# Optimization experiments

Measured on AMD Instinct MI355X. Metric: run time of the kernel, lower is better.

The kernel has to match this reference:

```python
import jax, jax.numpy as jnp
import numpy as np

S = 9                      # spiral length
V = [8192, 4096, 2048, 1024, 512]  # verts per level, finest -> latent


def grid_sample_bilinear(feat, grid):
    # feat [B,C,H,W], grid [B,P,2] in [-1,1]; bilinear, align_corners=True
    B, C, H, W = feat.shape
    x = (grid[..., 0] + 1.0) * 0.5 * (W - 1)
    y = (grid[..., 1] + 1.0) * 0.5 * (H - 1)
    x0 = jnp.floor(x); y0 = jnp.floor(y)
    wx = x - x0; wy = y - y0
    x0i = jnp.clip(x0.astype(jnp.int32), 0, W - 1)
    x1i = jnp.clip(x0.astype(jnp.int32) + 1, 0, W - 1)
    y0i = jnp.clip(y0.astype(jnp.int32), 0, H - 1)
    y1i = jnp.clip(y0.astype(jnp.int32) + 1, 0, H - 1)
    featf = feat.reshape(B, C, H * W).transpose(0, 2, 1)  # [B,HW,C]
    def gat(yi, xi):
        return jnp.take_along_axis(featf, (yi * W + xi)[..., None], axis=1)  # [B,P,C]
    w00 = ((1 - wy) * (1 - wx))[..., None]
    w01 = ((1 - wy) * wx)[..., None]
    w10 = (wy * (1 - wx))[..., None]
    w11 = (wy * wx)[..., None]
    return gat(y0i, x0i) * w00 + gat(y0i, x1i) * w01 + gat(y1i, x0i) * w10 + gat(y1i, x1i) * w11


def pool(x, row, col, val):
    # sparse mesh upsample: gather cols, scale, scatter-add into rows
    n_out = row.shape[0] // 3
    g = x[:, col, :] * val[None, :, None]                       # [B,nnz,C]
    return jnp.zeros((x.shape[0], n_out, x.shape[-1]), x.dtype).at[:, row, :].add(g)


def dsconv(x, idx, wd, wp, b):
    # depthwise-separable spiral conv: gather spiral ring, depthwise over S, pointwise mix
    g = x[:, idx]                                # [B,N,S,C]
    dw = jnp.einsum('bnsc,sc->bnc', g, wd)       # depthwise over spiral dim
    return jnp.einsum('bnc,co->bno', dw, wp) + b # pointwise


def _forward(uv, feat, upsample, s0, s1, s2, s3,
             row0, col0, val0, row1, col1, val1, row2, col2, val2, row3, col3, val3,
             wd0, wp0, b0, wd1, wp1, b1, wd2, wp2, b2, wd3, wp3, b3, wdh, wph, bh):
    uvc = jnp.clip((uv - 0.5) * 2.0, -1.0, 1.0)
    x = grid_sample_bilinear(feat, uvc)           # [B,P,C]  (torch: [B,C,P] then permute)
    x = jnp.einsum('vp,bpc->bvc', upsample, x)    # [B,V4,C] latent mesh features
    x = jax.nn.relu(dsconv(pool(x, row3, col3, val3), s3, wd0, wp0, b0))  # [B,1024,512]
    x = jax.nn.relu(dsconv(pool(x, row2, col2, val2), s2, wd1, wp1, b1))  # [B,2048,256]
    x = jax.nn.relu(dsconv(pool(x, row1, col1, val1), s1, wd2, wp2, b2))  # [B,4096,128]
    x = jax.nn.relu(dsconv(pool(x, row0, col0, val0), s0, wd3, wp3, b3))  # [B,8192,64]
    return dsconv(x, s0, wdh, wph, bh)            # [B,8192,3]


def setup_inputs():
    ks = jax.random.split(jax.random.key(0), 64)
    B, P, C, H, W = 8, 21, 512, 32, 32
    inp = {}
    inp['uv'] = jax.random.uniform(ks[0], (B, P, 2), jnp.float32)
    inp['feat'] = jax.random.normal(ks[1], (B, C, H, W), jnp.float32)
    inp['upsample'] = 0.01 * jnp.ones((V[4], P), jnp.float32)
    for i in range(4):
        inp[f's{i}'] = jax.random.randint(ks[2 + i], (V[i], S), 0, V[i])
    for i in range(4):
        nnz = 3 * V[i]
        inp[f'row{i}'] = jax.random.randint(ks[6 + 3 * i], (nnz,), 0, V[i])
        inp[f'col{i}'] = jax.random.randint(ks[7 + 3 * i], (nnz,), 0, V[i + 1])
        inp[f'val{i}'] = jax.random.uniform(ks[8 + 3 * i], (nnz,), jnp.float32)
    chans = [(512, 512), (512, 256), (256, 128), (128, 64), (64, 3)]
    names = ['0', '1', '2', '3', 'h']
    k = 20
    for (ci, co), nm in zip(chans, names):
        inp[f'wd{nm}'] = 0.1 * jax.random.normal(ks[k], (S, ci), jnp.float32); k += 1
        inp[f'wp{nm}'] = jax.random.normal(ks[k], (ci, co), jnp.float32) * (1.0 / float(np.sqrt(ci))); k += 1
        inp[f'b{nm}'] = jnp.zeros((co,), jnp.float32); k += 1
    return inp


def reference(uv, feat, upsample, s0, s1, s2, s3,
              row0, col0, val0, row1, col1, val1, row2, col2, val2, row3, col3, val3,
              wd0, wp0, b0, wd1, wp1, b1, wd2, wp2, b2, wd3, wp3, b3, wdh, wph, bh):
    return _forward(uv, feat, upsample, s0, s1, s2, s3,
                    row0, col0, val0, row1, col1, val1, row2, col2, val2, row3, col3, val3,
                    wd0, wp0, b0, wd1, wp1, b1, wd2, wp2, b2, wd3, wp3, b3, wdh, wph, bh)
```

## Files before the change

### kernel.cpp

```cpp
#include <hip/hip_runtime.h>

#define B_  8
#define P_  21
#define H_  32
#define W_  32

typedef float f32x4 __attribute__((ext_vector_type(4)));
typedef _Float16 f16x8 __attribute__((ext_vector_type(8)));

struct CsrParams {
  const int*   row[4];
  const int*   col[4];
  const float* val[4];
  int*   cnt[4];
  int*   rowptr[4];
  int*   colsout[4];
  float* valsout[4];
  int    nnz[4];
  int    V[4];
};

__global__ void count_kernel(CsrParams p) {
  int l = blockIdx.y;
  int k = blockIdx.x * 256 + threadIdx.x;
  if (k < p.nnz[l]) atomicAdd(&p.cnt[l][p.row[l][k]], 1);
}

__global__ void scan_kernel(CsrParams p) {
  int l = blockIdx.x;
  int V = p.V[l];
  int* cnt = p.cnt[l];
  int* rp  = p.rowptr[l];
  int t = threadIdx.x;
  int chunk = V / 256;
  int base = t * chunk;
  int s = 0;
  for (int i = 0; i < chunk; ++i) s += cnt[base + i];
  __shared__ int sm[256];
  sm[t] = s;
  __syncthreads();
  for (int off = 1; off < 256; off <<= 1) {
    int v = (t >= off) ? sm[t - off] : 0;
    __syncthreads();
    sm[t] += v;
    __syncthreads();
  }
  int run = sm[t] - s;
  for (int i = 0; i < chunk; ++i) {
    int c = cnt[base + i];
    rp[base + i]  = run;
    cnt[base + i] = run;
    run += c;
  }
  if (t == 255) rp[V] = run;
}

__global__ void fill_kernel(CsrParams p) {
  int l = blockIdx.y;
  int k = blockIdx.x * 256 + threadIdx.x;
  if (k < p.nnz[l]) {
    int r = p.row[l][k];
    int pos = atomicAdd(&p.cnt[l][r], 1);
    p.colsout[l][pos] = p.col[l][k];
    p.valsout[l][pos] = p.val[l][k];
  }
}

__global__ void sample_kernel(const float* __restrict__ uv,
                              const float* __restrict__ feat,
                              float* __restrict__ xs) {
  int bp = blockIdx.x;
  int b  = bp / P_;
  float u0 = uv[bp * 2 + 0], u1 = uv[bp * 2 + 1];
  float gx = fminf(fmaxf((u0 - 0.5f) * 2.0f, -1.0f), 1.0f);
  float gy = fminf(fmaxf((u1 - 0.5f) * 2.0f, -1.0f), 1.0f);
  float fx = (gx + 1.0f) * 0.5f * (W_ - 1);
  float fy = (gy + 1.0f) * 0.5f * (H_ - 1);
  float x0f = floorf(fx), y0f = floorf(fy);
  float wx = fx - x0f, wy = fy - y0f;
  int x0 = (int)x0f, y0 = (int)y0f;
  int x0i = min(max(x0, 0), W_ - 1), x1i = min(max(x0 + 1, 0), W_ - 1);
  int y0i = min(max(y0, 0), H_ - 1), y1i = min(max(y0 + 1, 0), H_ - 1);
  float w00 = (1.f - wy) * (1.f - wx), w01 = (1.f - wy) * wx;
  float w10 = wy * (1.f - wx),        w11 = wy * wx;
  for (int c = threadIdx.x; c < 512; c += blockDim.x) {
    const float* fb = feat + ((size_t)(b * 512 + c)) * (H_ * W_);
    float v = fb[y0i * W_ + x0i] * w00 + fb[y0i * W_ + x1i] * w01 +
              fb[y1i * W_ + x0i] * w10 + fb[y1i * W_ + x1i] * w11;
    xs[(size_t)bp * 512 + c] = v;
  }
}

__global__ void upsample_kernel(const float* __restrict__ up,
                                const float* __restrict__ xs,
                                float* __restrict__ xu) {
  int v = blockIdx.x, b = blockIdx.y;
  int c4 = threadIdx.x << 2;
  float4 acc = make_float4(0.f, 0.f, 0.f, 0.f);
  for (int p = 0; p < P_; ++p) {
    float u = up[v * P_ + p];
    const float4 xv = *(const float4*)&xs[((size_t)(b * P_ + p)) * 512 + c4];
    acc.x = fmaf(u, xv.x, acc.x);
    acc.y = fmaf(u, xv.y, acc.y);
    acc.z = fmaf(u, xv.z, acc.z);
    acc.w = fmaf(u, xv.w, acc.w);
  }
  *(float4*)&xu[((size_t)(b * 512 + v)) * 512 + c4] = acc;
}

__global__ __launch_bounds__(256) void pool_kernel(
    const float* __restrict__ x,
    const int* __restrict__ rowptr,
    const int* __restrict__ cols,
    const float* __restrict__ vals,
    float* __restrict__ out,
    int Vout, int Vin, int Cin) {
  const int lpr    = Cin >> 3;
  const int lshift = 31 - __clz(lpr);
  const int rpb    = 256 >> lshift;
  const int lr = threadIdx.x >> lshift;
  const int lc = threadIdx.x & (lpr - 1);
  const int b  = blockIdx.x & 7;
  const int n  = (blockIdx.x >> 3) * rpb + lr;
  const int c8 = lc << 3;
  const float* xb = x + (size_t)b * Vin * Cin + c8;
  int j0 = rowptr[n], j1 = rowptr[n + 1];
  float4 a0 = make_float4(0.f, 0.f, 0.f, 0.f);
  float4 a1 = make_float4(0.f, 0.f, 0.f, 0.f);
  for (int j = j0; j < j1; ++j) {
    float v = vals[j];
    const float* xr = xb + (size_t)cols[j] * Cin;
    float4 x0 = *(const float4*)xr;
    float4 x1 = *(const float4*)(xr + 4);
    a0.x = fmaf(v, x0.x, a0.x); a0.y = fmaf(v, x0.y, a0.y);
    a0.z = fmaf(v, x0.z, a0.z); a0.w = fmaf(v, x0.w, a0.w);
    a1.x = fmaf(v, x1.x, a1.x); a1.y = fmaf(v, x1.y, a1.y);
    a1.z = fmaf(v, x1.z, a1.z); a1.w = fmaf(v, x1.w, a1.w);
  }
  float* op = &out[((size_t)b * Vout + n) * Cin + c8];
  *(float4*)op = a0;
  *(float4*)(op + 4) = a1;
}

__global__ __launch_bounds__(256) void dw_split_kernel(
    const float* __restrict__ xin,
    const int* __restrict__ sidx,
    const float* __restrict__ wd,
    _Float16* __restrict__ a0o,
    _Float16* __restrict__ a1o,
    int Vout, int Cin) {
  const int lpr    = Cin >> 3;
  const int lshift = 31 - __clz(lpr);
  const int rpb    = 256 >> lshift;
  const int lr = threadIdx.x >> lshift;
  const int lc = threadIdx.x & (lpr - 1);
  const int b  = blockIdx.x & 7;
  const int n  = (blockIdx.x >> 3) * rpb + lr;
  const int c8 = lc << 3;
  const float* xb = xin + (size_t)b * Vout * Cin + c8;

  int idx[9];
  #pragma unroll
  for (int s = 0; s < 9; ++s) idx[s] = sidx[n * 9 + s];

  float4 a0 = make_float4(0.f, 0.f, 0.f, 0.f);
  float4 a1 = make_float4(0.f, 0.f, 0.f, 0.f);
  #pragma unroll
  for (int s = 0; s < 9; ++s) {
    const float* xr = xb + (size_t)idx[s] * Cin;
    float4 x0 = *(const float4*)xr;
    float4 x1 = *(const float4*)(xr + 4);
    const float* wr = wd + s * Cin + c8;
    float4 w0 = *(const float4*)wr;
    float4 w1 = *(const float4*)(wr + 4);
    a0.x = fmaf(w0.x, x0.x, a0.x); a0.y = fmaf(w0.y, x0.y, a0.y);
    a0.z = fmaf(w0.z, x0.z, a0.z); a0.w = fmaf(w0.w, x0.w, a0.w);
    a1.x = fmaf(w1.x, x1.x, a1.x); a1.y = fmaf(w1.y, x1.y, a1.y);
    a1.z = fmaf(w1.z, x1.z, a1.z); a1.w = fmaf(w1.w, x1.w, a1.w);
  }

  size_t m = (size_t)b * Vout + n;
  float v[8] = {a0.x, a0.y, a0.z, a0.w, a1.x, a1.y, a1.z, a1.w};
  f16x8 hi, lo;
  #pragma unroll
  for (int i = 0; i < 8; ++i) {
    _Float16 h0 = (_Float16)v[i];
    float r = (v[i] - (float)h0) * 2048.0f;
    hi[i] = h0;
    lo[i] = (_Float16)r;
  }
  *(f16x8*)&a0o[m * Cin + c8] = hi;
  *(f16x8*)&a1o[m * Cin + c8] = lo;
}

struct BsplitParams {
  const float* wp[4];
  int K[4], N[4], off[4];
  _Float16* b0;
  _Float16* b1;
};

__global__ void bsplit_all_kernel(BsplitParams p) {
  int idx = blockIdx.x * 256 + threadIdx.x;
  #pragma unroll
  for (int t = 0; t < 4; ++t) {
    int sz = p.N[t] * p.K[t];
    if (idx < sz) {
      int n = idx / p.K[t], k = idx - n * p.K[t];
      float v = p.wp[t][(size_t)k * p.N[t] + n];
      _Float16 h0 = (_Float16)v;
      float r = (v - (float)h0) * 2048.0f;
      p.b0[p.off[t] + idx] = h0;
      p.b1[p.off[t] + idx] = (_Float16)r;
      return;
    }
    idx -= sz;
  }
}

__global__ __launch_bounds__(256) void gemm_f16x2(
    const _Float16* __restrict__ A0, const _Float16* __restrict__ A1,
    const _Float16* __restrict__ Bt0, const _Float16* __restrict__ Bt1,
    const float* __restrict__ bias, float* __restrict__ C,
    int M, int N, int K) {
  constexpr int RP = 72;
  __shared__ _Float16 As[2][128][RP];
  __shared__ _Float16 Bs[2][64][RP];
  const int tid = threadIdx.x;
  const int bx = blockIdx.x;
  const int xr_ = (bx & 7) * (gridDim.x >> 3) + (bx >> 3);
  const int m0 = xr_ * 128, n0 = blockIdx.y * 64;
  const int wid = tid >> 6, lane = tid & 63;
  const int wr = wid >> 1, wc = wid & 1;
  const int lo = lane & 15, hi = lane >> 4;

  f32x4 accM[4][2], accC[4][2];
  #pragma unroll
  for (int mi = 0; mi < 4; ++mi)
    #pragma unroll
    for (int nj = 0; nj < 2; ++nj) {
      accM[mi][nj] = (f32x4){0.f, 0.f, 0.f, 0.f};
      accC[mi][nj] = (f32x4){0.f, 0.f, 0.f, 0.f};
    }

  const _Float16* gA[2] = {A0, A1};
  const _Float16* gB[2] = {Bt0, Bt1};

  for (int k0 = 0; k0 < K; k0 += 64) {
    #pragma unroll
    for (int p = 0; p < 2; ++p) {
      #pragma unroll
      for (int i = 0; i < 4; ++i) {
        int c = tid + 256 * i;
        int r = c >> 3, k8 = (c & 7) << 3;
        uint4 v = *(const uint4*)(gA[p] + (size_t)(m0 + r) * K + k0 + k8);
        *(uint4*)&As[p][r][k8] = v;
      }
      #pragma unroll
      for (int i = 0; i < 2; ++i) {
        int c = tid + 256 * i;
        int r = c >> 3, k8 = (c & 7) << 3;
        uint4 v = *(const uint4*)(gB[p] + (size_t)(n0 + r) * K + k0 + k8);
        *(uint4*)&Bs[p][r][k8] = v;
      }
    }
    __syncthreads();
    #pragma unroll
    for (int s = 0; s < 2; ++s) {
      const int kk = s * 32 + hi * 8;
      f16x8 af[4][2], bf[2][2];
      #pragma unroll
      for (int mi = 0; mi < 4; ++mi) {
        af[mi][0] = *(const f16x8*)&As[0][wr * 64 + mi * 16 + lo][kk];
        af[mi][1] = *(const f16x8*)&As[1][wr * 64 + mi * 16 + lo][kk];
      }
      #pragma unroll
      for (int nj = 0; nj < 2; ++nj) {
        bf[nj][0] = *(const f16x8*)&Bs[0][wc * 32 + nj * 16 + lo][kk];
        bf[nj][1] = *(const f16x8*)&Bs[1][wc * 32 + nj * 16 + lo][kk];
      }
      #pragma unroll
      for (int mi = 0; mi < 4; ++mi)
        #pragma unroll
        for (int nj = 0; nj < 2; ++nj) {
          accM[mi][nj] = __builtin_amdgcn_mfma_f32_16x16x32_f16(
              af[mi][0], bf[nj][0], accM[mi][nj], 0, 0, 0);
          accC[mi][nj] = __builtin_amdgcn_mfma_f32_16x16x32_f16(
              af[mi][0], bf[nj][1], accC[mi][nj], 0, 0, 0);
          accC[mi][nj] = __builtin_amdgcn_mfma_f32_16x16x32_f16(
              af[mi][1], bf[nj][0], accC[mi][nj], 0, 0, 0);
        }
    }
    __syncthreads();
  }

  const float INV = 1.0f / 2048.0f;
  #pragma unroll
  for (int mi = 0; mi < 4; ++mi)
    #pragma unroll
    for (int nj = 0; nj < 2; ++nj) {
      int col = n0 + wc * 32 + nj * 16 + lo;
      float bv = bias[col];
      #pragma unroll
      for (int r = 0; r < 4; ++r) {
        int row = m0 + wr * 64 + mi * 16 + hi * 4 + r;
        float v = accM[mi][nj][r] + accC[mi][nj][r] * INV + bv;
        v = fmaxf(v, 0.f);
        C[(size_t)row * N + col] = v;
      }
    }
}

__global__ __launch_bounds__(256) void head_fused_kernel(
    const float* __restrict__ x,
    const int* __restrict__ sidx,
    const float* __restrict__ wdh,
    const float* __restrict__ wph,
    const float* __restrict__ bh,
    float* __restrict__ out) {
  const int bid  = blockIdx.x;
  const int b    = bid & 7;
  const int wid  = threadIdx.x >> 6;
  const int lane = threadIdx.x & 63;
  const int n    = (bid >> 3) * 4 + wid;
  const float* xb = x + (size_t)b * 8192 * 64 + lane;

  int idx[9];
  #pragma unroll
  for (int s = 0; s < 9; ++s) idx[s] = sidx[n * 9 + s];

  float acc = 0.f;
  #pragma unroll
  for (int s = 0; s < 9; ++s)
    acc = fmaf(wdh[s * 64 + lane], xb[(size_t)idx[s] * 64], acc);

  float a0 = acc * wph[lane * 3 + 0];
  float a1 = acc * wph[lane * 3 + 1];
  float a2 = acc * wph[lane * 3 + 2];
  for (int off = 32; off > 0; off >>= 1) {
    a0 += __shfl_down(a0, off);
    a1 += __shfl_down(a1, off);
    a2 += __shfl_down(a2, off);
  }
  if (lane == 0) {
    size_t row = (size_t)b * 8192 + n;
    out[row * 3 + 0] = a0 + bh[0];
    out[row * 3 + 1] = a1 + bh[1];
    out[row * 3 + 2] = a2 + bh[2];
  }
}

extern "C" void kernel_launch(void* const* d_in, const int* in_sizes, int n_in,
                              void* d_out, int out_size, void* d_ws, size_t ws_size,
                              hipStream_t stream) {
  const float* uv   = (const float*)d_in[0];
  const float* feat = (const float*)d_in[1];
  const float* up   = (const float*)d_in[2];
  const int* sArr[4] = {(const int*)d_in[3], (const int*)d_in[4],
                        (const int*)d_in[5], (const int*)d_in[6]};

  const size_t SLAB = 8ull * 2048 * 512;
  float* Wf = (float*)d_ws;
  float* S0 = Wf;
  float* S1 = Wf + SLAB;
  _Float16* A0 = (_Float16*)(S1 + SLAB);
  _Float16* A1 = A0 + SLAB;
  _Float16* Bt0all = (_Float16*)(S0 + 4500000);
  _Float16* Bt1all = Bt0all + 434176;
  float* xs = (float*)(A1 + SLAB);
  int* ib = (int*)(xs + (size_t)B_ * P_ * 512);

  int Vt[4] = {1024, 2048, 4096, 8192};
  int NZ[4] = {3072, 6144, 12288, 24576};
  int* cnt[4]; int* rp[4]; int* co[4]; float* va[4];
  {
    int* pc = ib;
    for (int t = 0; t < 4; ++t) { cnt[t] = pc; pc += Vt[t]; }
    for (int t = 0; t < 4; ++t) { rp[t] = pc; pc += Vt[t] + 1; }
    for (int t = 0; t < 4; ++t) { co[t] = pc; pc += NZ[t]; }
    float* pv = (float*)pc;
    for (int t = 0; t < 4; ++t) { va[t] = pv; pv += NZ[t]; }
  }

  CsrParams cp;
  for (int t = 0; t < 4; ++t) {
    int i = 3 - t;
    cp.row[t] = (const int*)d_in[7 + 3 * i];
    cp.col[t] = (const int*)d_in[8 + 3 * i];
    cp.val[t] = (const float*)d_in[9 + 3 * i];
    cp.cnt[t] = cnt[t]; cp.rowptr[t] = rp[t];
    cp.colsout[t] = co[t]; cp.valsout[t] = va[t];
    cp.nnz[t] = NZ[t]; cp.V[t] = Vt[t];
  }

  hipMemsetAsync(ib, 0, 15360 * sizeof(int), stream);
  count_kernel<<<dim3(96, 4), 256, 0, stream>>>(cp);
  scan_kernel<<<4, 256, 0, stream>>>(cp);
  fill_kernel<<<dim3(96, 4), 256, 0, stream>>>(cp);

  sample_kernel<<<B_ * P_, 256, 0, stream>>>(uv, feat, xs);
  upsample_kernel<<<dim3(512, B_), 128, 0, stream>>>(up, xs, S0);

  struct Stg { int Vin, Vout, Cin, Cout; const int* s; const float *wd, *wp, *bias; };
  Stg st[4] = {
    {512, 1024, 512, 512, sArr[3], (const float*)d_in[19], (const float*)d_in[20], (const float*)d_in[21]},
    {1024, 2048, 512, 256, sArr[2], (const float*)d_in[22], (const float*)d_in[23], (const float*)d_in[24]},
    {2048, 4096, 256, 128, sArr[1], (const float*)d_in[25], (const float*)d_in[26], (const float*)d_in[27]},
    {4096, 8192, 128, 64, sArr[0], (const float*)d_in[28], (const float*)d_in[29], (const float*)d_in[30]},
  };

  BsplitParams bp;
  int boff = 0;
  for (int t = 0; t < 4; ++t) {
    bp.wp[t] = st[t].wp;
    bp.K[t] = st[t].Cin; bp.N[t] = st[t].Cout;
    bp.off[t] = boff;
    boff += st[t].Cin * st[t].Cout;
  }
  bp.b0 = Bt0all; bp.b1 = Bt1all;
  bsplit_all_kernel<<<(boff + 255) / 256, 256, 0, stream>>>(bp);

  for (int t = 0; t < 4; ++t) {
    int rpb = 2048 / st[t].Cin;
    pool_kernel<<<8 * (st[t].Vout / rpb), 256, 0, stream>>>(
        S0, rp[t], co[t], va[t], S1, st[t].Vout, st[t].Vin, st[t].Cin);
    dw_split_kernel<<<8 * (st[t].Vout / rpb), 256, 0, stream>>>(
        S1, st[t].s, st[t].wd, A0, A1, st[t].Vout, st[t].Cin);
    int M = B_ * st[t].Vout;
    gemm_f16x2<<<dim3(M / 128, st[t].Cout / 64), 256, 0, stream>>>(
        A0, A1, Bt0all + bp.off[t], Bt1all + bp.off[t],
        st[t].bias, S0, M, st[t].Cout, st[t].Cin);
  }

  head_fused_kernel<<<8 * (8192 / 4), 256, 0, stream>>>(
      S0, sArr[0], (const float*)d_in[31], (const float*)d_in[32],
      (const float*)d_in[33], (float*)d_out);
}
```

Before: 280.1 us.

## Widen GEMM N-tile to 128 and process two vertices per thread in depthwise kernel

The GEMM is templated on its N-tile width. Layers with at least 128 output channels now use 128-wide tiles, so each loaded A tile is reused across more MFMAs, at the cost of more accumulator registers; launch bounds now request two blocks per CU. The depthwise split kernel handles two vertices per thread (n and n + Vout/2) with half the grid. This adds memory-level parallelism for the gathers but doubles register use per thread.

```diff
diff --git a/kernel.cpp b/kernel.cpp
--- a/kernel.cpp
+++ b/kernel.cpp
@@ -156,20 +156,28 @@
   const int lc = threadIdx.x & (lpr - 1);
   const int b  = blockIdx.x & 7;
   const int n  = (blockIdx.x >> 3) * rpb + lr;
+  const int n2 = n + (Vout >> 1);
   const int c8 = lc << 3;
   const float* xb = xin + (size_t)b * Vout * Cin + c8;
 
-  int idx[9];
-  #pragma unroll
-  for (int s = 0; s < 9; ++s) idx[s] = sidx[n * 9 + s];
+  int idx[9], idx2[9];
+  #pragma unroll
+  for (int s = 0; s < 9; ++s) idx[s]  = sidx[n * 9 + s];
+  #pragma unroll
+  for (int s = 0; s < 9; ++s) idx2[s] = sidx[n2 * 9 + s];
 
   float4 a0 = make_float4(0.f, 0.f, 0.f, 0.f);
   float4 a1 = make_float4(0.f, 0.f, 0.f, 0.f);
+  float4 c0 = make_float4(0.f, 0.f, 0.f, 0.f);
+  float4 c1 = make_float4(0.f, 0.f, 0.f, 0.f);
   #pragma unroll
   for (int s = 0; s < 9; ++s) {
-    const float* xr = xb + (size_t)idx[s] * Cin;
+    const float* xr  = xb + (size_t)idx[s]  * Cin;
+    const float* xr2 = xb + (size_t)idx2[s] * Cin;
     float4 x0 = *(const float4*)xr;
     float4 x1 = *(const float4*)(xr + 4);
+    float4 y0 = *(const float4*)xr2;
+    float4 y1 = *(const float4*)(xr2 + 4);
     const float* wr = wd + s * Cin + c8;
     float4 w0 = *(const float4*)wr;
     float4 w1 = *(const float4*)(wr + 4);
@@ -177,20 +185,30 @@
     a0.z = fmaf(w0.z, x0.z, a0.z); a0.w = fmaf(w0.w, x0.w, a0.w);
     a1.x = fmaf(w1.x, x1.x, a1.x); a1.y = fmaf(w1.y, x1.y, a1.y);
     a1.z = fmaf(w1.z, x1.z, a1.z); a1.w = fmaf(w1.w, x1.w, a1.w);
-  }
-
-  size_t m = (size_t)b * Vout + n;
-  float v[8] = {a0.x, a0.y, a0.z, a0.w, a1.x, a1.y, a1.z, a1.w};
-  f16x8 hi, lo;
+    c0.x = fmaf(w0.x, y0.x, c0.x); c0.y = fmaf(w0.y, y0.y, c0.y);
+    c0.z = fmaf(w0.z, y0.z, c0.z); c0.w = fmaf(w0.w, y0.w, c0.w);
+    c1.x = fmaf(w1.x, y1.x, c1.x); c1.y = fmaf(w1.y, y1.y, c1.y);
+    c1.z = fmaf(w1.z, y1.z, c1.z); c1.w = fmaf(w1.w, y1.w, c1.w);
+  }
+
+  size_t m  = (size_t)b * Vout + n;
+  size_t m2 = (size_t)b * Vout + n2;
+  float va[8] = {a0.x, a0.y, a0.z, a0.w, a1.x, a1.y, a1.z, a1.w};
+  float vc[8] = {c0.x, c0.y, c0.z, c0.w, c1.x, c1.y, c1.z, c1.w};
+  f16x8 hiA, loA, hiC, loC;
   #pragma unroll
   for (int i = 0; i < 8; ++i) {
-    _Float16 h0 = (_Float16)v[i];
-    float r = (v[i] - (float)h0) * 2048.0f;
-    hi[i] = h0;
-    lo[i] = (_Float16)r;
-  }
-  *(f16x8*)&a0o[m * Cin + c8] = hi;
-  *(f16x8*)&a1o[m * Cin + c8] = lo;
+    _Float16 h0 = (_Float16)va[i];
+    float r = (va[i] - (float)h0) * 2048.0f;
+    hiA[i] = h0; loA[i] = (_Float16)r;
+    _Float16 h1 = (_Float16)vc[i];
+    float r2 = (vc[i] - (float)h1) * 2048.0f;
+    hiC[i] = h1; loC[i] = (_Float16)r2;
+  }
+  *(f16x8*)&a0o[m  * Cin + c8] = hiA;
+  *(f16x8*)&a1o[m  * Cin + c8] = loA;
+  *(f16x8*)&a0o[m2 * Cin + c8] = hiC;
+  *(f16x8*)&a1o[m2 * Cin + c8] = loC;
 }
 
 struct BsplitParams {
@@ -218,27 +236,29 @@
   }
 }
 
-__global__ __launch_bounds__(256) void gemm_f16x2(
+template <int BN>
+__global__ __launch_bounds__(256, 2) void gemm_f16x2(
     const _Float16* __restrict__ A0, const _Float16* __restrict__ A1,
     const _Float16* __restrict__ Bt0, const _Float16* __restrict__ Bt1,
     const float* __restrict__ bias, float* __restrict__ C,
     int M, int N, int K) {
   constexpr int RP = 72;
+  constexpr int NR = BN / 32;
   __shared__ _Float16 As[2][128][RP];
-  __shared__ _Float16 Bs[2][64][RP];
+  __shared__ _Float16 Bs[2][BN][RP];
   const int tid = threadIdx.x;
   const int bx = blockIdx.x;
   const int xr_ = (bx & 7) * (gridDim.x >> 3) + (bx >> 3);
-  const int m0 = xr_ * 128, n0 = blockIdx.y * 64;
+  const int m0 = xr_ * 128, n0 = blockIdx.y * BN;
   const int wid = tid >> 6, lane = tid & 63;
   const int wr = wid >> 1, wc = wid & 1;
   const int lo = lane & 15, hi = lane >> 4;
 
-  f32x4 accM[4][2], accC[4][2];
+  f32x4 accM[4][NR], accC[4][NR];
   #pragma unroll
   for (int mi = 0; mi < 4; ++mi)
     #pragma unroll
-    for (int nj = 0; nj < 2; ++nj) {
+    for (int nj = 0; nj < NR; ++nj) {
       accM[mi][nj] = (f32x4){0.f, 0.f, 0.f, 0.f};
       accC[mi][nj] = (f32x4){0.f, 0.f, 0.f, 0.f};
     }
@@ -257,7 +277,7 @@
         *(uint4*)&As[p][r][k8] = v;
       }
       #pragma unroll
-      for (int i = 0; i < 2; ++i) {
+      for (int i = 0; i < BN / 32; ++i) {
         int c = tid + 256 * i;
         int r = c >> 3, k8 = (c & 7) << 3;
         uint4 v = *(const uint4*)(gB[p] + (size_t)(n0 + r) * K + k0 + k8);
@@ -268,21 +288,21 @@
     #pragma unroll
     for (int s = 0; s < 2; ++s) {
       const int kk = s * 32 + hi * 8;
-      f16x8 af[4][2], bf[2][2];
+      f16x8 af[4][2], bf[NR][2];
       #pragma unroll
       for (int mi = 0; mi < 4; ++mi) {
         af[mi][0] = *(const f16x8*)&As[0][wr * 64 + mi * 16 + lo][kk];
         af[mi][1] = *(const f16x8*)&As[1][wr * 64 + mi * 16 + lo][kk];
       }
       #pragma unroll
-      for (int nj = 0; nj < 2; ++nj) {
-        bf[nj][0] = *(const f16x8*)&Bs[0][wc * 32 + nj * 16 + lo][kk];
-        bf[nj][1] = *(const f16x8*)&Bs[1][wc * 32 + nj * 16 + lo][kk];
+      for (int nj = 0; nj < NR; ++nj) {
+        bf[nj][0] = *(const f16x8*)&Bs[0][wc * (BN / 2) + nj * 16 + lo][kk];
+        bf[nj][1] = *(const f16x8*)&Bs[1][wc * (BN / 2) + nj * 16 + lo][kk];
       }
       #pragma unroll
       for (int mi = 0; mi < 4; ++mi)
         #pragma unroll
-        for (int nj = 0; nj < 2; ++nj) {
+        for (int nj = 0; nj < NR; ++nj) {
           accM[mi][nj] = __builtin_amdgcn_mfma_f32_16x16x32_f16(
               af[mi][0], bf[nj][0], accM[mi][nj], 0, 0, 0);
           accC[mi][nj] = __builtin_amdgcn_mfma_f32_16x16x32_f16(
@@ -298,8 +318,8 @@
   #pragma unroll
   for (int mi = 0; mi < 4; ++mi)
     #pragma unroll
-    for (int nj = 0; nj < 2; ++nj) {
-      int col = n0 + wc * 32 + nj * 16 + lo;
+    for (int nj = 0; nj < NR; ++nj) {
+      int col = n0 + wc * (BN / 2) + nj * 16 + lo;
       float bv = bias[col];
       #pragma unroll
       for (int r = 0; r < 4; ++r) {
@@ -424,12 +444,18 @@
     int rpb = 2048 / st[t].Cin;
     pool_kernel<<<8 * (st[t].Vout / rpb), 256, 0, stream>>>(
         S0, rp[t], co[t], va[t], S1, st[t].Vout, st[t].Vin, st[t].Cin);
-    dw_split_kernel<<<8 * (st[t].Vout / rpb), 256, 0, stream>>>(
+    dw_split_kernel<<<8 * (st[t].Vout / 2 / rpb), 256, 0, stream>>>(
         S1, st[t].s, st[t].wd, A0, A1, st[t].Vout, st[t].Cin);
     int M = B_ * st[t].Vout;
-    gemm_f16x2<<<dim3(M / 128, st[t].Cout / 64), 256, 0, stream>>>(
-        A0, A1, Bt0all + bp.off[t], Bt1all + bp.off[t],
-        st[t].bias, S0, M, st[t].Cout, st[t].Cin);
+    if (st[t].Cout >= 128) {
+      gemm_f16x2<128><<<dim3(M / 128, st[t].Cout / 128), 256, 0, stream>>>(
+          A0, A1, Bt0all + bp.off[t], Bt1all + bp.off[t],
+          st[t].bias, S0, M, st[t].Cout, st[t].Cin);
+    } else {
+      gemm_f16x2<64><<<dim3(M / 128, st[t].Cout / 64), 256, 0, stream>>>(
+          A0, A1, Bt0all + bp.off[t], Bt1all + bp.off[t],
+          st[t].bias, S0, M, st[t].Cout, st[t].Cin);
+    }
   }
 
   head_fused_kernel<<<8 * (8192 / 4), 256, 0, stream>>>(
```

Measured after the change: 306.4 us. 1.09x slower.
